# Kernel optimization log

Measured on AMD Instinct MI355X. Metric: run time of the kernel, lower is better.

The kernel has to match this reference:

```python
import jax, jax.numpy as jnp
import numpy as np

THRESH = 0.999  # dynamic outlier percentile

# Standard NF4 signpost values (normalized to [-1, 1])
NF4 = np.array([-1.0, -0.6961928009986877, -0.5250730514526367, -0.39491748809814453,
                -0.28444138169288635, -0.18477343022823334, -0.09105003625154495, 0.0,
                0.07958029955625534, 0.16093020141124725, 0.24611230194568634, 0.33791524171829224,
                0.44070982933044434, 0.5626170039176941, 0.7229568362236023, 1.0], dtype=np.float32)


def setup_inputs() -> dict:
    key = jax.random.key(0)
    k1, k2 = jax.random.split(key)
    x = jax.random.normal(k1, (4096, 4096), dtype=jnp.float32)        # [tokens, in_features]
    weight = jax.random.normal(k2, (4096, 4096), dtype=jnp.float32)   # [out_features, in_features]
    nf_lut = jnp.asarray(NF4)                                          # [16] NF4 poles
    return {"x": x, "weight": weight, "nf_lut": nf_lut}


def quantize_nf(weight, nf_lut):
    # --- dynamic outlier detection (get_outliers_dynamic, qchannel=-1) ---
    t = 1.0 - (1.0 - THRESH) / 2.0
    upper = jnp.quantile(weight, t, axis=-1, keepdims=True)        # [R,1]
    lower = jnp.quantile(weight, 1.0 - t, axis=-1, keepdims=True)  # [R,1]
    outlier_mask = (weight <= lower) | (weight >= upper)           # [R,C] bool

    # --- include_sparse scale computation (quant_fn_nf) ---
    outliers0 = weight * outlier_mask
    median = jnp.median(weight, axis=-1, keepdims=True)
    tmp = weight - outliers0 + median * outlier_mask               # outliers replaced by median
    maxval = jnp.max(tmp, axis=-1, keepdims=True)
    minval = jnp.min(tmp, axis=-1, keepdims=True)
    offset = (maxval + minval) * 0.5
    rangeval = (maxval - minval) * 0.5

    w = weight - offset
    outliers = w * outlier_mask        # sparse (fp) component
    w = w - outliers                   # dense component
    w_scaled = w / rangeval            # normalized to ~[-1, 1]

    # --- nearest-pole (NF) rounding: argmin over |w - pole| ---
    idx = jnp.argmin(jnp.abs(w_scaled[..., None] - nf_lut), axis=-1)  # [R,C]
    Q = nf_lut[idx].astype(jnp.float16).astype(jnp.float32)           # .half() in torch

    # --- dequant ---
    qw = Q * rangeval + outliers + offset
    qw = jnp.nan_to_num(qw, nan=0.0, posinf=0.0, neginf=0.0)
    return qw


def reference(x, weight, nf_lut):
    qweight = quantize_nf(weight, nf_lut)   # simulated NF4 dense+sparse dequant
    return x @ qweight.T                    # [tokens, out_features]
```

## Files before the change

### kernel.cpp

```cpp
#include <hip/hip_runtime.h>
#include <hip/hip_fp16.h>
#include <stdint.h>

typedef __attribute__((ext_vector_type(4))) float f32x4;
typedef __attribute__((ext_vector_type(8))) short short8;

__device__ __forceinline__ unsigned short f2bf(float f) {
  unsigned int b = __float_as_uint(f);
  b = b + 0x7FFFu + ((b >> 16) & 1u);
  return (unsigned short)(b >> 16);
}

#define CE(a, b) { float _lo = fminf((a), (b)), _hi = fmaxf((a), (b)); (a) = _lo; (b) = _hi; }

__device__ __forceinline__ void merge8(float x[8]) {
  CE(x[0], x[4]); CE(x[1], x[5]); CE(x[2], x[6]); CE(x[3], x[7]);
  CE(x[2], x[4]); CE(x[3], x[5]);
  CE(x[1], x[2]); CE(x[3], x[4]); CE(x[5], x[6]);
}

__global__ __launch_bounds__(256) void prep_kernel(const float* __restrict__ x,
                                                   const float* __restrict__ W,
                                                   const float* __restrict__ lut,
                                                   unsigned short* __restrict__ xb,
                                                   unsigned short* __restrict__ qb) {
  const int tid = threadIdx.x;

  if (blockIdx.x >= 4096) {
    int b = blockIdx.x - 4096;
    int base = b * 1024 + tid;
#pragma unroll
    for (int it = 0; it < 4; ++it) {
      int i = base + it * 256;
      f32x4 v = ((const f32x4*)x)[i];
      ushort4 u;
      u.x = f2bf(v[0]); u.y = f2bf(v[1]); u.z = f2bf(v[2]); u.w = f2bf(v[3]);
      ((ushort4*)xb)[i] = u;
    }
    return;
  }

  const int C = 4096;
  const int row = blockIdx.x;
  const int lane = tid & 63;
  const int wv = tid >> 6;

  __shared__ float s_lutf[16];
  __shared__ float s_luth[16];
  __shared__ float s_red[4][8];
  __shared__ float s_par[4];

  if (tid < 16) {
    float f = lut[tid];
    s_lutf[tid] = f;
    s_luth[tid] = __half2float(__float2half(f));
  }

  const f32x4* Wp = (const f32x4*)(W + (size_t)row * C);
  f32x4 v[4];
#pragma unroll
  for (int i = 0; i < 4; ++i) v[i] = Wp[i * 256 + tid];

  float bot[4] = {__builtin_inff(), __builtin_inff(), __builtin_inff(), __builtin_inff()};
  float top[4] = {-__builtin_inff(), -__builtin_inff(), -__builtin_inff(), -__builtin_inff()};
#pragma unroll
  for (int i = 0; i < 4; ++i) {
#pragma unroll
    for (int j = 0; j < 4; ++j) {
      float f = v[i][j];
      bot[3] = fminf(bot[3], f); CE(bot[2], bot[3]); CE(bot[1], bot[2]); CE(bot[0], bot[1]);
      top[0] = fmaxf(top[0], f); CE(top[0], top[1]); CE(top[1], top[2]); CE(top[2], top[3]);
    }
  }

#pragma unroll
  for (int d = 1; d < 64; d <<= 1) {
    float xx[8];
#pragma unroll
    for (int j = 0; j < 4; ++j) { xx[j] = bot[j]; xx[4 + j] = __shfl_xor(bot[j], d); }
    merge8(xx);
#pragma unroll
    for (int j = 0; j < 4; ++j) bot[j] = xx[j];
#pragma unroll
    for (int j = 0; j < 4; ++j) { xx[j] = top[j]; xx[4 + j] = __shfl_xor(top[j], d); }
    merge8(xx);
#pragma unroll
    for (int j = 0; j < 4; ++j) top[j] = xx[4 + j];
  }

  if (lane == 0) {
#pragma unroll
    for (int j = 0; j < 4; ++j) { s_red[wv][j] = bot[j]; s_red[wv][4 + j] = top[j]; }
  }
  __syncthreads();

  if (tid == 0) {
    float a[8], b[8], m[8];
#pragma unroll
    for (int j = 0; j < 4; ++j) { a[j] = s_red[0][j]; a[4 + j] = s_red[1][j]; }
    merge8(a);
#pragma unroll
    for (int j = 0; j < 4; ++j) { b[j] = s_red[2][j]; b[4 + j] = s_red[3][j]; }
    merge8(b);
#pragma unroll
    for (int j = 0; j < 4; ++j) { m[j] = a[j]; m[4 + j] = b[j]; }
    merge8(m);
    float lower = m[2] + 0.0475f * (m[3] - m[2]);
#pragma unroll
    for (int j = 0; j < 4; ++j) { a[j] = s_red[0][4 + j]; a[4 + j] = s_red[1][4 + j]; }
    merge8(a);
#pragma unroll
    for (int j = 0; j < 4; ++j) { b[j] = s_red[2][4 + j]; b[4 + j] = s_red[3][4 + j]; }
    merge8(b);
#pragma unroll
    for (int j = 0; j < 4; ++j) { m[j] = a[4 + j]; m[4 + j] = b[4 + j]; }
    merge8(m);
    float upper = m[4] + 0.9525f * (m[5] - m[4]);
    s_par[0] = lower; s_par[1] = upper;
  }
  __syncthreads();

  float lower = s_par[0], upper = s_par[1];

  float mn = __builtin_inff(), mx = -__builtin_inff();
#pragma unroll
  for (int i = 0; i < 4; ++i) {
#pragma unroll
    for (int j = 0; j < 4; ++j) {
      float f = v[i][j];
      bool outl = (f <= lower) || (f >= upper);
      if (!outl) { mn = fminf(mn, f); mx = fmaxf(mx, f); }
    }
  }
#pragma unroll
  for (int d = 1; d < 64; d <<= 1) {
    mn = fminf(mn, __shfl_xor(mn, d));
    mx = fmaxf(mx, __shfl_xor(mx, d));
  }
  if (lane == 0) { s_red[wv][0] = mn; s_red[wv][1] = mx; }
  __syncthreads();
  if (tid == 0) {
    float tmn = fminf(fminf(s_red[0][0], s_red[1][0]), fminf(s_red[2][0], s_red[3][0]));
    float tmx = fmaxf(fmaxf(s_red[0][1], s_red[1][1]), fmaxf(s_red[2][1], s_red[3][1]));
    s_par[2] = (tmx + tmn) * 0.5f;
    s_par[3] = (tmx - tmn) * 0.5f;
  }
  __syncthreads();
  float offset = s_par[2], range = s_par[3];

  unsigned short* outr = qb + (size_t)row * C;
#pragma unroll
  for (int i = 0; i < 4; ++i) {
    ushort4 o;
    unsigned short os[4];
#pragma unroll
    for (int j = 0; j < 4; ++j) {
      float f = v[i][j];
      bool outl = (f <= lower) || (f >= upper);
      float q;
      if (outl) {
        q = f;
      } else {
        float ws = (f - offset) / range;
        float best = fabsf(ws - s_lutf[0]);
        int bi = 0;
#pragma unroll
        for (int t = 1; t < 16; ++t) {
          float d2 = fabsf(ws - s_lutf[t]);
          if (d2 < best) { best = d2; bi = t; }
        }
        q = s_luth[bi] * range + offset;
      }
      if (!isfinite(q)) q = 0.0f;
      os[j] = f2bf(q);
    }
    o.x = os[0]; o.y = os[1]; o.z = os[2]; o.w = os[3];
    ((ushort4*)outr)[i * 256 + tid] = o;
  }
}

#define GK 4096

__device__ __forceinline__ void gload16(const void* gp, void* lp) {
  __builtin_amdgcn_global_load_lds(
      (const __attribute__((address_space(1))) unsigned int*)(uintptr_t)gp,
      (__attribute__((address_space(3))) unsigned int*)(unsigned int)(uintptr_t)lp,
      16, 0, 0);
}

__global__ __launch_bounds__(512, 2) void gemm_bt(const unsigned short* __restrict__ A,
                                                  const unsigned short* __restrict__ B,
                                                  float* __restrict__ C) {
  __shared__ __align__(16) unsigned short sA[4][8192];
  __shared__ __align__(16) unsigned short sB[4][8192];

  const int tid = threadIdx.x;
  const int lane = tid & 63;
  const int wv = tid >> 6;
  const int wm = wv >> 2, wn = wv & 3;
  const int fr = lane & 15, fk = lane >> 4;

  int bi = blockIdx.x;
  int swz = (bi & 7) * 32 + (bi >> 3);
  int brow = swz >> 4, bcol = swz & 15;

  const unsigned short* Abase = A + (size_t)brow * 256 * GK;
  const unsigned short* Bbase = B + (size_t)bcol * 256 * GK;

  const int fkx = (fk * 16) ^ ((fr & 0xC) << 2);

  f32x4 acc[8][4];
#pragma unroll
  for (int m = 0; m < 8; ++m)
#pragma unroll
    for (int n = 0; n < 4; ++n) acc[m][n] = (f32x4){0.f, 0.f, 0.f, 0.f};

  auto stage = [&](const unsigned short* gb, unsigned short (*sbuf)[8192], int slot, int g) {
    int kt = g >> 1;
    if (kt >= 64) kt = 0;
    int k0 = (kt << 6) + ((g & 1) << 5);
#pragma unroll
    for (int l = 0; l < 2; ++l) {
      int Lb = ((wv * 2 + l) << 10) + lane * 16;
      int r = Lb >> 6;
      int cb = (Lb & 63) ^ ((r & 0xC) << 2);
      gload16(gb + (size_t)r * GK + k0 + (cb >> 1), (char*)&sbuf[slot][0] + Lb);
    }
  };

  stage(Abase, sA, 0, 0);
  stage(Bbase, sB, 0, 0);
  stage(Abase, sA, 1, 1);
  stage(Bbase, sB, 1, 1);
  asm volatile("s_waitcnt vmcnt(4)" ::: "memory");
  __builtin_amdgcn_s_barrier();
  __builtin_amdgcn_sched_barrier(0);

#pragma unroll 1
  for (int i = 0; i < 32; ++i) {
#pragma unroll
    for (int q = 0; q < 4; ++q) {
      const char* sAq = (const char*)&sA[q][0];
      const char* sBq = (const char*)&sB[q][0];
      short8 af[4], bfr[4];

#pragma unroll
      for (int m = 0; m < 4; ++m)
        af[m] = *(const short8*)(sAq + (wm * 128 + m * 16 + fr) * 64 + fkx);
#pragma unroll
      for (int n = 0; n < 4; ++n)
        bfr[n] = *(const short8*)(sBq + (wn * 64 + n * 16 + fr) * 64 + fkx);
      stage(Abase, sA, (q + 2) & 3, 4 * i + q + 2);
      __builtin_amdgcn_s_barrier();
      asm volatile("s_waitcnt lgkmcnt(0)" ::: "memory");
      __builtin_amdgcn_sched_barrier(0);
      __builtin_amdgcn_s_setprio(1);
#pragma unroll
      for (int m = 0; m < 4; ++m)
#pragma unroll
        for (int n = 0; n < 4; ++n)
          acc[m][n] = __builtin_amdgcn_mfma_f32_16x16x32_bf16(af[m], bfr[n], acc[m][n], 0, 0, 0);
      __builtin_amdgcn_s_setprio(0);
      __builtin_amdgcn_sched_barrier(0);
      __builtin_amdgcn_s_barrier();

#pragma unroll
      for (int m = 0; m < 4; ++m)
        af[m] = *(const short8*)(sAq + (wm * 128 + (4 + m) * 16 + fr) * 64 + fkx);
      stage(Bbase, sB, (q + 2) & 3, 4 * i + q + 2);
      __builtin_amdgcn_s_barrier();
      asm volatile("s_waitcnt lgkmcnt(0)" ::: "memory");
      __builtin_amdgcn_sched_barrier(0);
      __builtin_amdgcn_s_setprio(1);
#pragma unroll
      for (int m = 0; m < 4; ++m)
#pragma unroll
        for (int n = 0; n < 4; ++n)
          acc[4 + m][n] = __builtin_amdgcn_mfma_f32_16x16x32_bf16(af[m], bfr[n], acc[4 + m][n], 0, 0, 0);
      __builtin_amdgcn_s_setprio(0);
      __builtin_amdgcn_sched_barrier(0);
      asm volatile("s_waitcnt vmcnt(4)" ::: "memory");
      __builtin_amdgcn_s_barrier();
      __builtin_amdgcn_sched_barrier(0);
    }
  }

  const int rbase = brow * 256 + wm * 128;
  const int cbase = bcol * 256 + wn * 64;
#pragma unroll
  for (int m = 0; m < 8; ++m)
#pragma unroll
    for (int n = 0; n < 4; ++n)
#pragma unroll
      for (int j = 0; j < 4; ++j) {
        int rr = rbase + m * 16 + fk * 4 + j;
        int cc = cbase + n * 16 + fr;
        C[(size_t)rr * GK + cc] = acc[m][n][j];
      }
}

extern "C" void kernel_launch(void* const* d_in, const int* in_sizes, int n_in,
                              void* d_out, int out_size, void* d_ws, size_t ws_size,
                              hipStream_t stream) {
  const float* x = (const float*)d_in[0];
  const float* W = (const float*)d_in[1];
  const float* lut = (const float*)d_in[2];
  float* out = (float*)d_out;

  unsigned short* xb = (unsigned short*)d_ws;
  unsigned short* qb = xb + (size_t)4096 * 4096;

  prep_kernel<<<8192, 256, 0, stream>>>(x, W, lut, xb, qb);
  gemm_bt<<<256, 512, 0, stream>>>(xb, qb, out);
}
```

Measured before the change: 179.1 us.

## Restructure GEMM main loop into half-tile staging with 64-wide K tiles

Shared-memory tiles are reorganized from four 32-wide K slots into double-buffered 64-wide K tiles split into two 128-row halves. The loop now stages each half separately and interleaves four MFMA quadrants (A-half by B-half) with the loads, so each fragment is reused across two quadrant passes and fewer barriers occur per K step. A new XOR swizzle on a 128-byte row stride replaces the old one. The intent is to cut LDS read traffic and barrier overhead per K step, at the cost of a more intricate schedule. The buffer-reuse ordering and the 'vmcnt(4)' waits must line up exactly with the new staging order to avoid races.

After: 173.8 us. 3.0% less time.

```diff
diff --git a/kernel.cpp b/kernel.cpp
--- a/kernel.cpp
+++ b/kernel.cpp
@@ -188,11 +188,18 @@
       16, 0, 0);
 }
 
+#define BAR()    __builtin_amdgcn_s_barrier()
+#define SCHED0() __builtin_amdgcn_sched_barrier(0)
+#define LGKM0()  asm volatile("s_waitcnt lgkmcnt(0)" ::: "memory")
+#define VM4()    asm volatile("s_waitcnt vmcnt(4)" ::: "memory")
+#define PRIO1()  __builtin_amdgcn_s_setprio(1)
+#define PRIO0()  __builtin_amdgcn_s_setprio(0)
+
 __global__ __launch_bounds__(512, 2) void gemm_bt(const unsigned short* __restrict__ A,
                                                   const unsigned short* __restrict__ B,
                                                   float* __restrict__ C) {
-  __shared__ __align__(16) unsigned short sA[4][8192];
-  __shared__ __align__(16) unsigned short sB[4][8192];
+  __shared__ __align__(16) unsigned short sA[2][2][8192];
+  __shared__ __align__(16) unsigned short sB[2][2][8192];
 
   const int tid = threadIdx.x;
   const int lane = tid & 63;
@@ -207,7 +214,18 @@
   const unsigned short* Abase = A + (size_t)brow * 256 * GK;
   const unsigned short* Bbase = B + (size_t)bcol * 256 * GK;
 
-  const int fkx = (fk * 16) ^ ((fr & 0xC) << 2);
+  const int c0 = (fk * 16) ^ (((fr >> 2) & 1) << 5);
+
+  const int srow = lane >> 3;
+  const int scolE = (((lane & 7) * 16) ^ (((lane >> 5) & 1) << 5)) >> 1;
+
+  auto stage = [&](const unsigned short* gb, unsigned short* lb, int h, int kt) {
+    const unsigned short* g = gb + ((size_t)h * 128) * GK + kt * 64 + scolE;
+    char* lc = (char*)lb + wv * 1024 + lane * 16;
+#pragma unroll
+    for (int l = 0; l < 2; ++l)
+      gload16(g + (size_t)(wv * 8 + l * 64 + srow) * GK, lc + l * 8192);
+  };
 
   f32x4 acc[8][4];
 #pragma unroll
@@ -215,73 +233,164 @@
 #pragma unroll
     for (int n = 0; n < 4; ++n) acc[m][n] = (f32x4){0.f, 0.f, 0.f, 0.f};
 
-  auto stage = [&](const unsigned short* gb, unsigned short (*sbuf)[8192], int slot, int g) {
-    int kt = g >> 1;
-    if (kt >= 64) kt = 0;
-    int k0 = (kt << 6) + ((g & 1) << 5);
-#pragma unroll
-    for (int l = 0; l < 2; ++l) {
-      int Lb = ((wv * 2 + l) << 10) + lane * 16;
-      int r = Lb >> 6;
-      int cb = (Lb & 63) ^ ((r & 0xC) << 2);
-      gload16(gb + (size_t)r * GK + k0 + (cb >> 1), (char*)&sbuf[slot][0] + Lb);
-    }
-  };
-
-  stage(Abase, sA, 0, 0);
-  stage(Bbase, sB, 0, 0);
-  stage(Abase, sA, 1, 1);
-  stage(Bbase, sB, 1, 1);
-  asm volatile("s_waitcnt vmcnt(4)" ::: "memory");
-  __builtin_amdgcn_s_barrier();
-  __builtin_amdgcn_sched_barrier(0);
+  stage(Abase, &sA[0][0][0], 0, 0);
+  stage(Abase, &sA[0][1][0], 1, 0);
+  stage(Bbase, &sB[0][0][0], 0, 0);
+  stage(Bbase, &sB[0][1][0], 1, 0);
+  stage(Bbase, &sB[1][0][0], 0, 1);
+  stage(Bbase, &sB[1][1][0], 1, 1);
+  VM4();
+  BAR();
+  SCHED0();
+
+  const int rB = (wn & 1) * 64;
 
 #pragma unroll 1
   for (int i = 0; i < 32; ++i) {
-#pragma unroll
-    for (int q = 0; q < 4; ++q) {
-      const char* sAq = (const char*)&sA[q][0];
-      const char* sBq = (const char*)&sB[q][0];
-      short8 af[4], bfr[4];
-
-#pragma unroll
-      for (int m = 0; m < 4; ++m)
-        af[m] = *(const short8*)(sAq + (wm * 128 + m * 16 + fr) * 64 + fkx);
-#pragma unroll
-      for (int n = 0; n < 4; ++n)
-        bfr[n] = *(const short8*)(sBq + (wn * 64 + n * 16 + fr) * 64 + fkx);
-      stage(Abase, sA, (q + 2) & 3, 4 * i + q + 2);
-      __builtin_amdgcn_s_barrier();
-      asm volatile("s_waitcnt lgkmcnt(0)" ::: "memory");
-      __builtin_amdgcn_sched_barrier(0);
-      __builtin_amdgcn_s_setprio(1);
-#pragma unroll
-      for (int m = 0; m < 4; ++m)
-#pragma unroll
-        for (int n = 0; n < 4; ++n)
-          acc[m][n] = __builtin_amdgcn_mfma_f32_16x16x32_bf16(af[m], bfr[n], acc[m][n], 0, 0, 0);
-      __builtin_amdgcn_s_setprio(0);
-      __builtin_amdgcn_sched_barrier(0);
-      __builtin_amdgcn_s_barrier();
-
-#pragma unroll
-      for (int m = 0; m < 4; ++m)
-        af[m] = *(const short8*)(sAq + (wm * 128 + (4 + m) * 16 + fr) * 64 + fkx);
-      stage(Bbase, sB, (q + 2) & 3, 4 * i + q + 2);
-      __builtin_amdgcn_s_barrier();
-      asm volatile("s_waitcnt lgkmcnt(0)" ::: "memory");
-      __builtin_amdgcn_sched_barrier(0);
-      __builtin_amdgcn_s_setprio(1);
-#pragma unroll
-      for (int m = 0; m < 4; ++m)
-#pragma unroll
-        for (int n = 0; n < 4; ++n)
-          acc[4 + m][n] = __builtin_amdgcn_mfma_f32_16x16x32_bf16(af[m], bfr[n], acc[4 + m][n], 0, 0, 0);
-      __builtin_amdgcn_s_setprio(0);
-      __builtin_amdgcn_sched_barrier(0);
-      asm volatile("s_waitcnt vmcnt(4)" ::: "memory");
-      __builtin_amdgcn_s_barrier();
-      __builtin_amdgcn_sched_barrier(0);
+    const int ktA1 = 2 * i + 1;
+    const int ktN0 = (2 * i + 2 < 64) ? 2 * i + 2 : 63;
+    const int ktN1 = (2 * i + 3 < 64) ? 2 * i + 3 : 63;
+
+    short8 af[4][2], bf0[2][2], bf1[2][2];
+
+    {
+      const char* bA = (const char*)&sA[0][wm][0];
+      const char* bB = (const char*)&sB[0][wn >> 1][0];
+
+#pragma unroll
+      for (int m = 0; m < 4; ++m)
+#pragma unroll
+        for (int kh = 0; kh < 2; ++kh)
+          af[m][kh] = *(const short8*)(bA + (m * 16 + fr) * 128 + kh * 64 + c0);
+#pragma unroll
+      for (int n = 0; n < 2; ++n)
+#pragma unroll
+        for (int kh = 0; kh < 2; ++kh)
+          bf0[n][kh] = *(const short8*)(bB + (rB + n * 16 + fr) * 128 + kh * 64 + c0);
+      stage(Abase, &sA[1][0][0], 0, ktA1);
+      BAR(); LGKM0(); SCHED0(); PRIO1();
+#pragma unroll
+      for (int m = 0; m < 4; ++m)
+#pragma unroll
+        for (int n = 0; n < 2; ++n)
+#pragma unroll
+          for (int kh = 0; kh < 2; ++kh)
+            acc[m][n] = __builtin_amdgcn_mfma_f32_16x16x32_bf16(af[m][kh], bf0[n][kh], acc[m][n], 0, 0, 0);
+      PRIO0(); SCHED0(); BAR();
+
+#pragma unroll
+      for (int n = 0; n < 2; ++n)
+#pragma unroll
+        for (int kh = 0; kh < 2; ++kh)
+          bf1[n][kh] = *(const short8*)(bB + (rB + (n + 2) * 16 + fr) * 128 + kh * 64 + c0);
+      stage(Abase, &sA[1][1][0], 1, ktA1);
+      BAR(); LGKM0(); SCHED0(); PRIO1();
+#pragma unroll
+      for (int m = 0; m < 4; ++m)
+#pragma unroll
+        for (int n = 0; n < 2; ++n)
+#pragma unroll
+          for (int kh = 0; kh < 2; ++kh)
+            acc[m][n + 2] = __builtin_amdgcn_mfma_f32_16x16x32_bf16(af[m][kh], bf1[n][kh], acc[m][n + 2], 0, 0, 0);
+      PRIO0(); SCHED0(); BAR();
+
+#pragma unroll
+      for (int m = 0; m < 4; ++m)
+#pragma unroll
+        for (int kh = 0; kh < 2; ++kh)
+          af[m][kh] = *(const short8*)(bA + ((m + 4) * 16 + fr) * 128 + kh * 64 + c0);
+      stage(Bbase, &sB[0][0][0], 0, ktN0);
+      BAR(); LGKM0(); SCHED0(); PRIO1();
+#pragma unroll
+      for (int m = 0; m < 4; ++m)
+#pragma unroll
+        for (int n = 0; n < 2; ++n)
+#pragma unroll
+          for (int kh = 0; kh < 2; ++kh)
+            acc[m + 4][n + 2] = __builtin_amdgcn_mfma_f32_16x16x32_bf16(af[m][kh], bf1[n][kh], acc[m + 4][n + 2], 0, 0, 0);
+      PRIO0(); SCHED0(); BAR();
+
+      stage(Bbase, &sB[0][1][0], 1, ktN0);
+      BAR(); PRIO1();
+#pragma unroll
+      for (int m = 0; m < 4; ++m)
+#pragma unroll
+        for (int n = 0; n < 2; ++n)
+#pragma unroll
+          for (int kh = 0; kh < 2; ++kh)
+            acc[m + 4][n] = __builtin_amdgcn_mfma_f32_16x16x32_bf16(af[m][kh], bf0[n][kh], acc[m + 4][n], 0, 0, 0);
+      PRIO0(); SCHED0();
+      VM4(); BAR(); SCHED0();
+    }
+
+    {
+      const char* bA = (const char*)&sA[1][wm][0];
+      const char* bB = (const char*)&sB[1][wn >> 1][0];
+
+#pragma unroll
+      for (int m = 0; m < 4; ++m)
+#pragma unroll
+        for (int kh = 0; kh < 2; ++kh)
+          af[m][kh] = *(const short8*)(bA + (m * 16 + fr) * 128 + kh * 64 + c0);
+#pragma unroll
+      for (int n = 0; n < 2; ++n)
+#pragma unroll
+        for (int kh = 0; kh < 2; ++kh)
+          bf0[n][kh] = *(const short8*)(bB + (rB + n * 16 + fr) * 128 + kh * 64 + c0);
+      stage(Abase, &sA[0][0][0], 0, ktN0);
+      BAR(); LGKM0(); SCHED0(); PRIO1();
+#pragma unroll
+      for (int m = 0; m < 4; ++m)
+#pragma unroll
+        for (int n = 0; n < 2; ++n)
+#pragma unroll
+          for (int kh = 0; kh < 2; ++kh)
+            acc[m][n] = __builtin_amdgcn_mfma_f32_16x16x32_bf16(af[m][kh], bf0[n][kh], acc[m][n], 0, 0, 0);
+      PRIO0(); SCHED0(); BAR();
+
+#pragma unroll
+      for (int n = 0; n < 2; ++n)
+#pragma unroll
+        for (int kh = 0; kh < 2; ++kh)
+          bf1[n][kh] = *(const short8*)(bB + (rB + (n + 2) * 16 + fr) * 128 + kh * 64 + c0);
+      stage(Abase, &sA[0][1][0], 1, ktN0);
+      BAR(); LGKM0(); SCHED0(); PRIO1();
+#pragma unroll
+      for (int m = 0; m < 4; ++m)
+#pragma unroll
+        for (int n = 0; n < 2; ++n)
+#pragma unroll
+          for (int kh = 0; kh < 2; ++kh)
+            acc[m][n + 2] = __builtin_amdgcn_mfma_f32_16x16x32_bf16(af[m][kh], bf1[n][kh], acc[m][n + 2], 0, 0, 0);
+      PRIO0(); SCHED0(); BAR();
+
+#pragma unroll
+      for (int m = 0; m < 4; ++m)
+#pragma unroll
+        for (int kh = 0; kh < 2; ++kh)
+          af[m][kh] = *(const short8*)(bA + ((m + 4) * 16 + fr) * 128 + kh * 64 + c0);
+      stage(Bbase, &sB[1][0][0], 0, ktN1);
+      BAR(); LGKM0(); SCHED0(); PRIO1();
+#pragma unroll
+      for (int m = 0; m < 4; ++m)
+#pragma unroll
+        for (int n = 0; n < 2; ++n)
+#pragma unroll
+          for (int kh = 0; kh < 2; ++kh)
+            acc[m + 4][n + 2] = __builtin_amdgcn_mfma_f32_16x16x32_bf16(af[m][kh], bf1[n][kh], acc[m + 4][n + 2], 0, 0, 0);
+      PRIO0(); SCHED0(); BAR();
+
+      stage(Bbase, &sB[1][1][0], 1, ktN1);
+      BAR(); PRIO1();
+#pragma unroll
+      for (int m = 0; m < 4; ++m)
+#pragma unroll
+        for (int n = 0; n < 2; ++n)
+#pragma unroll
+          for (int kh = 0; kh < 2; ++kh)
+            acc[m + 4][n] = __builtin_amdgcn_mfma_f32_16x16x32_bf16(af[m][kh], bf0[n][kh], acc[m + 4][n], 0, 0, 0);
+      PRIO0(); SCHED0();
+      VM4(); BAR(); SCHED0();
     }
   }
 
```
